# Kernel optimization log

Hardware: AMD Instinct MI355X
Metric: run time of the kernel (lower is better)

Reference implementation:

```python
import jax, jax.numpy as jnp
import numpy as np

N, M, F = 16384, 16384, 512
NUM_BATCHES = 16


def setup_inputs() -> dict:
    key = jax.random.key(0)
    k1, k2, k3, k4 = jax.random.split(key, 4)
    H_q = jax.random.normal(k1, (N, F), dtype=jnp.float32)
    H_c = jax.random.normal(k2, (M, F), dtype=jnp.float32)
    batch_q = jnp.sort(jax.random.randint(k3, (N,), 0, NUM_BATCHES, dtype=jnp.int64))
    batch_c = jnp.sort(jax.random.randint(k4, (M,), 0, NUM_BATCHES, dtype=jnp.int64))
    return {"H_q": H_q, "H_c": H_c, "batch_q": batch_q, "batch_c": batch_c}


def reference(H_q, H_c, batch_q, batch_c):
    # scores: [n, m] dense dot-product similarity
    scores = jnp.matmul(H_q, H_c.T)
    # mask[i, j] = True iff query i and candidate j belong to the same batch element
    mask = batch_q[:, None] == batch_c[None, :]
    out = jnp.where(mask, scores, -jnp.inf)
    return out, mask
```

## Files before the change

kernel.cpp:

```cpp
#include <hip/hip_runtime.h>
#include <hip/hip_bf16.h>
#include <math.h>


#define BM 128
#define BN 128
#define NEG_BIG (-3.3895313892515355e+38f)

typedef float    f32x4  __attribute__((ext_vector_type(4)));
typedef unsigned u32x4  __attribute__((ext_vector_type(4)));
typedef short    short8 __attribute__((ext_vector_type(8)));

__device__ __forceinline__ unsigned pk2(float a, float b) {
    unsigned ua = __builtin_bit_cast(unsigned, a);
    unsigned ub = __builtin_bit_cast(unsigned, b);
    return (ub & 0xFFFF0000u) | (ua >> 16);
}

__global__ __launch_bounds__(256) void dot_tile_kernel(
    const float* __restrict__ Hq, const float* __restrict__ Hc,
    const int* __restrict__ bq, const int* __restrict__ bc,
    float* __restrict__ out, float* __restrict__ mask_out,
    int M, int F, int ntx, int write_mask)
{
    const int t   = threadIdx.x;
    const int bid = blockIdx.x;
    const int i0  = (bid / ntx) * BM;
    const int j0  = (bid % ntx) * BN;

    if (!(bq[i0] <= bc[j0 + BN - 1] && bc[j0] <= bq[i0 + BM - 1])) {
        const f32x4 m4 = (f32x4){NEG_BIG, NEG_BIG, NEG_BIG, NEG_BIG};
        const f32x4 z4 = (f32x4){0.f, 0.f, 0.f, 0.f};
        #pragma unroll
        for (int v = 0; v < 16; ++v) {
            const int idx = t + v * 256;
            const int r   = idx >> 5;
            const int c4  = idx & 31;
            const size_t off = (size_t)(i0 + r) * M + j0 + c4 * 4;
            *(f32x4*)(out + off) = m4;
            if (write_mask) *(f32x4*)(mask_out + off) = z4;
        }
        return;
    }

    __shared__ short Abf[128 * 32];
    __shared__ short Bbf[128 * 32];
    __shared__ int bql[BM];
    __shared__ int bcl[BN];

    if (t < BM) bql[t] = bq[i0 + t];
    else        bcl[t - BM] = bc[j0 + (t - BM)];

    f32x4 acc[4][4];
    #pragma unroll
    for (int a = 0; a < 4; ++a)
        #pragma unroll
        for (int b = 0; b < 4; ++b) acc[a][b] = (f32x4){0.f, 0.f, 0.f, 0.f};

    const int l   = t & 63;
    const int wid = t >> 6;
    const int wr  = wid >> 1;
    const int wc  = wid & 1;
    const int lg  = l >> 4;
    const int lm  = l & 15;

    const int sr  = t >> 1;
    const int scf = (t & 1) * 16;
    const int swW = ((sr >> 1) & 3) << 4;
    const int wb0 = sr * 64 + (t & 1) * 32;
    const int swR = ((lm >> 1) & 3) << 4;

    const float* aptr = Hq + (size_t)(i0 + sr) * F + scf;
    const float* bptr = Hc + (size_t)(j0 + sr) * F + scf;

    char* Ab = (char*)Abf;
    char* Bb = (char*)Bbf;

    for (int ks = 0; ks < 16; ++ks) {
        const int k0 = ks * 32;
        f32x4 a0 = *(const f32x4*)(aptr + k0);
        f32x4 a1 = *(const f32x4*)(aptr + k0 + 4);
        f32x4 a2 = *(const f32x4*)(aptr + k0 + 8);
        f32x4 a3 = *(const f32x4*)(aptr + k0 + 12);
        f32x4 b0 = *(const f32x4*)(bptr + k0);
        f32x4 b1 = *(const f32x4*)(bptr + k0 + 4);
        f32x4 b2 = *(const f32x4*)(bptr + k0 + 8);
        f32x4 b3 = *(const f32x4*)(bptr + k0 + 12);
        __syncthreads();
        u32x4 pa0 = (u32x4){pk2(a0[0],a0[1]), pk2(a0[2],a0[3]), pk2(a1[0],a1[1]), pk2(a1[2],a1[3])};
        u32x4 pa1 = (u32x4){pk2(a2[0],a2[1]), pk2(a2[2],a2[3]), pk2(a3[0],a3[1]), pk2(a3[2],a3[3])};
        u32x4 pb0 = (u32x4){pk2(b0[0],b0[1]), pk2(b0[2],b0[3]), pk2(b1[0],b1[1]), pk2(b1[2],b1[3])};
        u32x4 pb1 = (u32x4){pk2(b2[0],b2[1]), pk2(b2[2],b2[3]), pk2(b3[0],b3[1]), pk2(b3[2],b3[3])};
        *(u32x4*)(Ab + ((wb0     ) ^ swW)) = pa0;
        *(u32x4*)(Ab + ((wb0 + 16) ^ swW)) = pa1;
        *(u32x4*)(Bb + ((wb0     ) ^ swW)) = pb0;
        *(u32x4*)(Bb + ((wb0 + 16) ^ swW)) = pb1;
        __syncthreads();
        short8 af[4], bf[4];
        #pragma unroll
        for (int m = 0; m < 4; ++m) {
            const int arow = wr * 64 + m * 16 + lm;
            af[m] = *(const short8*)(Ab + arow * 64 + ((lg * 16) ^ swR));
            const int brow = wc * 64 + m * 16 + lm;
            bf[m] = *(const short8*)(Bb + brow * 64 + ((lg * 16) ^ swR));
        }
        #pragma unroll
        for (int m = 0; m < 4; ++m)
            #pragma unroll
            for (int n = 0; n < 4; ++n)
                acc[m][n] = __builtin_amdgcn_mfma_f32_16x16x32_bf16(
                    af[m], bf[n], acc[m][n], 0, 0, 0);
    }

    #pragma unroll
    for (int m = 0; m < 4; ++m) {
        #pragma unroll
        for (int v = 0; v < 4; ++v) {
            const int rit = wr * 64 + m * 16 + lg * 4 + v;
            const int bqv = bql[rit];
            const size_t rowoff = (size_t)(i0 + rit) * M + j0;
            #pragma unroll
            for (int n = 0; n < 4; ++n) {
                const int cit = wc * 64 + n * 16 + lm;
                const bool eq = (bqv == bcl[cit]);
                out[rowoff + cit] = eq ? acc[m][n][v] : NEG_BIG;
                if (write_mask) mask_out[rowoff + cit] = eq ? 1.0f : 0.0f;
            }
        }
    }
}

extern "C" void kernel_launch(void* const* d_in, const int* in_sizes, int n_in,
                              void* d_out, int out_size, void* d_ws, size_t ws_size,
                              hipStream_t stream) {
    const float* Hq = (const float*)d_in[0];
    const float* Hc = (const float*)d_in[1];
    const int*   bq = (const int*)d_in[2];
    const int*   bc = (const int*)d_in[3];

    const int N = in_sizes[2];
    const int M = in_sizes[3];
    const int F = in_sizes[0] / N;

    float* out = (float*)d_out;
    const long long NM = (long long)N * M;
    const int write_mask = ((long long)out_size >= 2 * NM) ? 1 : 0;
    float* mask_out = out + NM;

    const int nty = N / BM;
    const int ntx = M / BN;

    dot_tile_kernel<<<nty * ntx, 256, 0, stream>>>(
        Hq, Hc, bq, bc, out, mask_out, M, F, ntx, write_mask);
}
```

Measured before the change: 467.7 us.

## Prefetch next K-slice into registers and stage epilogue through LDS for vector stores

Result: slower. 481.1 us (+2.9%).

```diff
diff --git a/kernel.cpp b/kernel.cpp
--- a/kernel.cpp
+++ b/kernel.cpp
@@ -43,10 +43,13 @@
         return;
     }
 
-    __shared__ short Abf[128 * 32];
-    __shared__ short Bbf[128 * 32];
+    __shared__ char SM[4 * 1088 * 4];
     __shared__ int bql[BM];
     __shared__ int bcl[BN];
+
+    char*  Ab = SM;
+    char*  Bb = SM + 8192;
+    float* tb = (float*)SM;
 
     if (t < BM) bql[t] = bq[i0 + t];
     else        bcl[t - BM] = bc[j0 + (t - BM)];
@@ -73,24 +76,36 @@
     const float* aptr = Hq + (size_t)(i0 + sr) * F + scf;
     const float* bptr = Hc + (size_t)(j0 + sr) * F + scf;
 
-    char* Ab = (char*)Abf;
-    char* Bb = (char*)Bbf;
+    const int nks = F >> 5;
 
-    for (int ks = 0; ks < 16; ++ks) {
-        const int k0 = ks * 32;
-        f32x4 a0 = *(const f32x4*)(aptr + k0);
-        f32x4 a1 = *(const f32x4*)(aptr + k0 + 4);
-        f32x4 a2 = *(const f32x4*)(aptr + k0 + 8);
-        f32x4 a3 = *(const f32x4*)(aptr + k0 + 12);
-        f32x4 b0 = *(const f32x4*)(bptr + k0);
-        f32x4 b1 = *(const f32x4*)(bptr + k0 + 4);
-        f32x4 b2 = *(const f32x4*)(bptr + k0 + 8);
-        f32x4 b3 = *(const f32x4*)(bptr + k0 + 12);
+    f32x4 cA[4], cB[4];
+    #pragma unroll
+    for (int u = 0; u < 4; ++u) {
+        cA[u] = *(const f32x4*)(aptr + u * 4);
+        cB[u] = *(const f32x4*)(bptr + u * 4);
+    }
+
+    #pragma unroll 2
+    for (int ks = 0; ks < nks; ++ks) {
+        f32x4 nA[4], nB[4];
+        const bool last = (ks == nks - 1);
+        if (!last) {
+            const int k1 = (ks + 1) * 32;
+            #pragma unroll
+            for (int u = 0; u < 4; ++u) {
+                nA[u] = *(const f32x4*)(aptr + k1 + u * 4);
+                nB[u] = *(const f32x4*)(bptr + k1 + u * 4);
+            }
+        }
         __syncthreads();
-        u32x4 pa0 = (u32x4){pk2(a0[0],a0[1]), pk2(a0[2],a0[3]), pk2(a1[0],a1[1]), pk2(a1[2],a1[3])};
-        u32x4 pa1 = (u32x4){pk2(a2[0],a2[1]), pk2(a2[2],a2[3]), pk2(a3[0],a3[1]), pk2(a3[2],a3[3])};
-        u32x4 pb0 = (u32x4){pk2(b0[0],b0[1]), pk2(b0[2],b0[3]), pk2(b1[0],b1[1]), pk2(b1[2],b1[3])};
-        u32x4 pb1 = (u32x4){pk2(b2[0],b2[1]), pk2(b2[2],b2[3]), pk2(b3[0],b3[1]), pk2(b3[2],b3[3])};
+        u32x4 pa0 = (u32x4){pk2(cA[0][0],cA[0][1]), pk2(cA[0][2],cA[0][3]),
+                            pk2(cA[1][0],cA[1][1]), pk2(cA[1][2],cA[1][3])};
+        u32x4 pa1 = (u32x4){pk2(cA[2][0],cA[2][1]), pk2(cA[2][2],cA[2][3]),
+                            pk2(cA[3][0],cA[3][1]), pk2(cA[3][2],cA[3][3])};
+        u32x4 pb0 = (u32x4){pk2(cB[0][0],cB[0][1]), pk2(cB[0][2],cB[0][3]),
+                            pk2(cB[1][0],cB[1][1]), pk2(cB[1][2],cB[1][3])};
+        u32x4 pb1 = (u32x4){pk2(cB[2][0],cB[2][1]), pk2(cB[2][2],cB[2][3]),
+                            pk2(cB[3][0],cB[3][1]), pk2(cB[3][2],cB[3][3])};
         *(u32x4*)(Ab + ((wb0     ) ^ swW)) = pa0;
         *(u32x4*)(Ab + ((wb0 + 16) ^ swW)) = pa1;
         *(u32x4*)(Bb + ((wb0     ) ^ swW)) = pb0;
@@ -110,23 +125,42 @@
             for (int n = 0; n < 4; ++n)
                 acc[m][n] = __builtin_amdgcn_mfma_f32_16x16x32_bf16(
                     af[m], bf[n], acc[m][n], 0, 0, 0);
+        if (!last) {
+            #pragma unroll
+            for (int u = 0; u < 4; ++u) { cA[u] = nA[u]; cB[u] = nB[u]; }
+        }
     }
 
+    __syncthreads();
+    const int r_loc = l >> 2;
+    const int sl    = l & 3;
     #pragma unroll
     for (int m = 0; m < 4; ++m) {
         #pragma unroll
-        for (int v = 0; v < 4; ++v) {
-            const int rit = wr * 64 + m * 16 + lg * 4 + v;
-            const int bqv = bql[rit];
-            const size_t rowoff = (size_t)(i0 + rit) * M + j0;
+        for (int n = 0; n < 4; ++n)
             #pragma unroll
-            for (int n = 0; n < 4; ++n) {
-                const int cit = wc * 64 + n * 16 + lm;
-                const bool eq = (bqv == bcl[cit]);
-                out[rowoff + cit] = eq ? acc[m][n][v] : NEG_BIG;
-                if (write_mask) mask_out[rowoff + cit] = eq ? 1.0f : 0.0f;
+            for (int v = 0; v < 4; ++v)
+                tb[wid * 1088 + (lg * 4 + v) * 68 + n * 16 + lm] = acc[m][n][v];
+        __syncthreads();
+        const int row = wr * 64 + m * 16 + r_loc;
+        const int bqv = bql[row];
+        const size_t rowoff = (size_t)(i0 + row) * M + j0;
+        #pragma unroll
+        for (int q = 0; q < 4; ++q) {
+            const int slot = sl + q * 4;
+            const int c    = wc * 64 + slot * 4;
+            f32x4 vv = *(f32x4*)&tb[wid * 1088 + r_loc * 68 + slot * 4];
+            f32x4 vo, vm;
+            #pragma unroll
+            for (int j = 0; j < 4; ++j) {
+                const bool eq = (bqv == bcl[c + j]);
+                vo[j] = eq ? vv[j] : NEG_BIG;
+                vm[j] = eq ? 1.0f : 0.0f;
             }
+            *(f32x4*)(out + rowoff + c) = vo;
+            if (write_mask) *(f32x4*)(mask_out + rowoff + c) = vm;
         }
+        __syncthreads();
     }
 }
 
```

## Pre-convert inputs to bf16 in workspace before the tiled matmul

Applied to the files above, without the earlier changes.

New measurement: 458.2 us. -2.0%, faster.

```diff
diff --git a/kernel.cpp b/kernel.cpp
--- a/kernel.cpp
+++ b/kernel.cpp
@@ -17,8 +17,31 @@
     return (ub & 0xFFFF0000u) | (ua >> 16);
 }
 
+__global__ __launch_bounds__(256) void cvt_kernel(
+    const float* __restrict__ Hq, const float* __restrict__ Hc,
+    unsigned short* __restrict__ q_bf, unsigned short* __restrict__ c_bf,
+    long long nq, long long ntot)
+{
+    const long long ng = ntot >> 3;
+    for (long long g = (long long)blockIdx.x * 256 + threadIdx.x; g < ng;
+         g += (long long)gridDim.x * 256) {
+        const long long base = g << 3;
+        const float* src;
+        unsigned short* dst;
+        if (base < nq) { src = Hq + base;        dst = q_bf + base; }
+        else           { src = Hc + (base - nq); dst = c_bf + (base - nq); }
+        f32x4 a = *(const f32x4*)(src);
+        f32x4 b = *(const f32x4*)(src + 4);
+        u32x4 p = (u32x4){pk2(a[0],a[1]), pk2(a[2],a[3]),
+                          pk2(b[0],b[1]), pk2(b[2],b[3])};
+        *(u32x4*)dst = p;
+    }
+}
+
+template <int USE_BF>
 __global__ __launch_bounds__(256) void dot_tile_kernel(
     const float* __restrict__ Hq, const float* __restrict__ Hc,
+    const unsigned short* __restrict__ Hq_bf, const unsigned short* __restrict__ Hc_bf,
     const int* __restrict__ bq, const int* __restrict__ bc,
     float* __restrict__ out, float* __restrict__ mask_out,
     int M, int F, int ntx, int write_mask)
@@ -64,33 +87,45 @@
     const int lg  = l >> 4;
     const int lm  = l & 15;
 
-    const int sr  = t >> 1;
-    const int scf = (t & 1) * 16;
+    const int sr   = t >> 1;
+    const int half = t & 1;
     const int swW = ((sr >> 1) & 3) << 4;
-    const int wb0 = sr * 64 + (t & 1) * 32;
+    const int wb0 = sr * 64 + half * 32;
     const int swR = ((lm >> 1) & 3) << 4;
-
-    const float* aptr = Hq + (size_t)(i0 + sr) * F + scf;
-    const float* bptr = Hc + (size_t)(j0 + sr) * F + scf;
 
     char* Ab = (char*)Abf;
     char* Bb = (char*)Bbf;
 
-    for (int ks = 0; ks < 16; ++ks) {
-        const int k0 = ks * 32;
-        f32x4 a0 = *(const f32x4*)(aptr + k0);
-        f32x4 a1 = *(const f32x4*)(aptr + k0 + 4);
-        f32x4 a2 = *(const f32x4*)(aptr + k0 + 8);
-        f32x4 a3 = *(const f32x4*)(aptr + k0 + 12);
-        f32x4 b0 = *(const f32x4*)(bptr + k0);
-        f32x4 b1 = *(const f32x4*)(bptr + k0 + 4);
-        f32x4 b2 = *(const f32x4*)(bptr + k0 + 8);
-        f32x4 b3 = *(const f32x4*)(bptr + k0 + 12);
+    const int nks = F >> 5;
+
+    const float* aptrf = Hq + (size_t)(i0 + sr) * F + half * 16;
+    const float* bptrf = Hc + (size_t)(j0 + sr) * F + half * 16;
+    const char*  aptrb = (const char*)Hq_bf + (size_t)(i0 + sr) * F * 2 + half * 32;
+    const char*  bptrb = (const char*)Hc_bf + (size_t)(j0 + sr) * F * 2 + half * 32;
+
+    for (int ks = 0; ks < nks; ++ks) {
+        u32x4 pa0, pa1, pb0, pb1;
+        if (USE_BF) {
+            pa0 = *(const u32x4*)(aptrb + ks * 64);
+            pa1 = *(const u32x4*)(aptrb + ks * 64 + 16);
+            pb0 = *(const u32x4*)(bptrb + ks * 64);
+            pb1 = *(const u32x4*)(bptrb + ks * 64 + 16);
+        } else {
+            const int k0 = ks * 32;
+            f32x4 a0 = *(const f32x4*)(aptrf + k0);
+            f32x4 a1 = *(const f32x4*)(aptrf + k0 + 4);
+            f32x4 a2 = *(const f32x4*)(aptrf + k0 + 8);
+            f32x4 a3 = *(const f32x4*)(aptrf + k0 + 12);
+            f32x4 b0 = *(const f32x4*)(bptrf + k0);
+            f32x4 b1 = *(const f32x4*)(bptrf + k0 + 4);
+            f32x4 b2 = *(const f32x4*)(bptrf + k0 + 8);
+            f32x4 b3 = *(const f32x4*)(bptrf + k0 + 12);
+            pa0 = (u32x4){pk2(a0[0],a0[1]), pk2(a0[2],a0[3]), pk2(a1[0],a1[1]), pk2(a1[2],a1[3])};
+            pa1 = (u32x4){pk2(a2[0],a2[1]), pk2(a2[2],a2[3]), pk2(a3[0],a3[1]), pk2(a3[2],a3[3])};
+            pb0 = (u32x4){pk2(b0[0],b0[1]), pk2(b0[2],b0[3]), pk2(b1[0],b1[1]), pk2(b1[2],b1[3])};
+            pb1 = (u32x4){pk2(b2[0],b2[1]), pk2(b2[2],b2[3]), pk2(b3[0],b3[1]), pk2(b3[2],b3[3])};
+        }
         __syncthreads();
-        u32x4 pa0 = (u32x4){pk2(a0[0],a0[1]), pk2(a0[2],a0[3]), pk2(a1[0],a1[1]), pk2(a1[2],a1[3])};
-        u32x4 pa1 = (u32x4){pk2(a2[0],a2[1]), pk2(a2[2],a2[3]), pk2(a3[0],a3[1]), pk2(a3[2],a3[3])};
-        u32x4 pb0 = (u32x4){pk2(b0[0],b0[1]), pk2(b0[2],b0[3]), pk2(b1[0],b1[1]), pk2(b1[2],b1[3])};
-        u32x4 pb1 = (u32x4){pk2(b2[0],b2[1]), pk2(b2[2],b2[3]), pk2(b3[0],b3[1]), pk2(b3[2],b3[3])};
         *(u32x4*)(Ab + ((wb0     ) ^ swW)) = pa0;
         *(u32x4*)(Ab + ((wb0 + 16) ^ swW)) = pa1;
         *(u32x4*)(Bb + ((wb0     ) ^ swW)) = pb0;
@@ -147,9 +182,22 @@
     const int write_mask = ((long long)out_size >= 2 * NM) ? 1 : 0;
     float* mask_out = out + NM;
 
+    const long long nq = (long long)N * F;
+    const long long nc = (long long)M * F;
+    const int use_bf = (ws_size >= (size_t)(nq + nc) * 2) ? 1 : 0;
+
+    unsigned short* q_bf = (unsigned short*)d_ws;
+    unsigned short* c_bf = q_bf + nq;
+
     const int nty = N / BM;
     const int ntx = M / BN;
 
-    dot_tile_kernel<<<nty * ntx, 256, 0, stream>>>(
-        Hq, Hc, bq, bc, out, mask_out, M, F, ntx, write_mask);
-}
+    if (use_bf) {
+        cvt_kernel<<<2048, 256, 0, stream>>>(Hq, Hc, q_bf, c_bf, nq, nq + nc);
+        dot_tile_kernel<1><<<nty * ntx, 256, 0, stream>>>(
+            Hq, Hc, q_bf, c_bf, bq, bc, out, mask_out, M, F, ntx, write_mask);
+    } else {
+        dot_tile_kernel<0><<<nty * ntx, 256, 0, stream>>>(
+            Hq, Hc, q_bf, c_bf, bq, bc, out, mask_out, M, F, ntx, write_mask);
+    }
+}
```
